# Kernel tuning notes

Hardware: AMD Instinct MI355X
Metric: run time of the kernel (lower is better)

Reference implementation:

```python
import jax, jax.numpy as jnp
import numpy as np

B, D, H, W = 16, 96, 96, 96
NUM_POINTS = 4096
THRESH = 0.5
CH = [3, 64, 128, 256, 512]   # shared-MLP channel progression (3 mlp layers + global_dim)
GROUPS = 8
EPS = 1e-5
HEAD_HIDDEN = 128


def setup_inputs() -> dict:
    key = jax.random.key(0)
    ks = jax.random.split(key, 8)
    inp = {"volume": jax.random.uniform(ks[0], (B, 1, D, H, W), jnp.float32)}
    for i in range(4):
        # Conv1d(kernel=1, no bias) weight (out, in); kaiming normal fan_out -> std=sqrt(2/out)
        inp[f"w{i+1}"] = jax.random.normal(ks[1 + i], (CH[i + 1], CH[i]), jnp.float32) * np.sqrt(2.0 / CH[i + 1]).astype(np.float32)
        inp[f"gn{i+1}_w"] = jnp.ones((CH[i + 1],), jnp.float32)
        inp[f"gn{i+1}_b"] = jnp.zeros((CH[i + 1],), jnp.float32)
    inp["fc1_w"] = jax.random.normal(ks[5], (HEAD_HIDDEN, CH[-1]), jnp.float32) * np.sqrt(2.0 / HEAD_HIDDEN).astype(np.float32)
    inp["fc1_b"] = jnp.zeros((HEAD_HIDDEN,), jnp.float32)
    inp["fc2_w"] = jax.random.normal(ks[6], (1, HEAD_HIDDEN), jnp.float32) * np.sqrt(2.0).astype(np.float32)
    inp["fc2_b"] = jnp.zeros((1,), jnp.float32)
    return inp


def volume_to_points(volume):
    """Batched, jit-safe version of volume_to_pointcloud (eval mode: linspace sampling)."""
    b, _, d, h, w = volume.shape
    mask = (volume[:, 0] > THRESH).reshape(b, -1)              # (B, D*H*W)
    n = mask.sum(axis=1)                                        # (B,) foreground counts
    # Stable argsort on ~mask puts foreground flat-indices first, in ascending order
    # == torch nonzero() ordering (row-major over D,H,W).
    order = jnp.argsort(jnp.logical_not(mask), axis=1, stable=True)  # (B, D*H*W)
    p = jnp.arange(NUM_POINTS)
    n_f = n.astype(jnp.float32)[:, None]
    # torch.linspace(0, n-1, P).long(): truncation toward zero
    lin = (p[None, :].astype(jnp.float32) * (n_f - 1.0) / (NUM_POINTS - 1)).astype(jnp.int32)
    lin = jnp.clip(lin, 0, jnp.maximum(n[:, None] - 1, 0))
    wrap = p[None, :] % jnp.maximum(n[:, None], 1)              # n < P fallback
    idx = jnp.where(n[:, None] >= NUM_POINTS, lin, wrap)        # (B, P)
    flat = jnp.take_along_axis(order, idx, axis=1)              # (B, P) flat voxel indices
    dd = flat // (h * w)
    hh = (flat // w) % h
    ww = flat % w
    coords = jnp.stack([dd, hh, ww], axis=1).astype(jnp.float32)  # (B, 3, P)
    scale = jnp.array([max(d - 1, 1), max(h - 1, 1), max(w - 1, 1)], jnp.float32)
    pts = coords / scale[None, :, None] * 2.0 - 1.0
    return jnp.where((n > 0)[:, None, None], pts, 0.0)


def group_norm(x, gamma, beta):
    b, c, npts = x.shape
    xg = x.reshape(b, GROUPS, c // GROUPS, npts)
    mu = xg.mean(axis=(2, 3), keepdims=True)
    var = xg.var(axis=(2, 3), keepdims=True)
    xn = ((xg - mu) * jax.lax.rsqrt(var + EPS)).reshape(b, c, npts)
    return xn * gamma[None, :, None] + beta[None, :, None]


def reference(volume, w1, gn1_w, gn1_b, w2, gn2_w, gn2_b, w3, gn3_w, gn3_b,
              w4, gn4_w, gn4_b, fc1_w, fc1_b, fc2_w, fc2_b):
    x = volume_to_points(volume)                                 # (B, 3, P)
    for cw, gw, gb in ((w1, gn1_w, gn1_b), (w2, gn2_w, gn2_b),
                       (w3, gn3_w, gn3_b), (w4, gn4_w, gn4_b)):
        x = jax.nn.relu(group_norm(jnp.einsum('oc,bcn->bon', cw, x), gw, gb))
    g = x.max(axis=2)                                            # (B, 512) global max-pool
    hdn = jax.nn.relu(g @ fc1_w.T + fc1_b)                       # dropout is identity in eval
    logits = (hdn @ fc2_w.T + fc2_b)[:, 0]                       # squeeze(-1) -> (B,)
    return logits
```

## Files before the change

kernel.cpp:

```cpp
#include <hip/hip_runtime.h>
#include <hip/hip_bf16.h>

#define NB 16
#define VOX 884736
#define NPTS 4096
#define CHUNK 1024
#define NCHUNK 864

typedef _Float16 f16x8 __attribute__((ext_vector_type(8)));
typedef _Float16 f16x4 __attribute__((ext_vector_type(4)));
typedef float f32x4 __attribute__((ext_vector_type(4)));

typedef const __attribute__((address_space(1))) _Float16 gf16;
typedef __attribute__((address_space(3))) _Float16 lf16;
#define GLOAD_LDS(gp, lp) __builtin_amdgcn_global_load_lds((gf16*)(gp), (lf16*)(lp), 16, 0, 0)

__device__ __forceinline__ f16x8 nrelu(f16x8 y, f16x8 sc, f16x8 sh) {
    f16x8 r = y * sc + sh;
    #pragma unroll
    for (int e = 0; e < 8; e++) r[e] = (r[e] > (_Float16)0.f) ? r[e] : (_Float16)0.f;
    return r;
}


__device__ inline void cast_chunk(const float* __restrict__ wf, _Float16* __restrict__ wh,
                                  int CIN, int t) {
    int lane = t & 63;
    int NCB = CIN / 32;
    int cb = (t >> 6) % NCB;
    int ob = t / (64 * NCB);
    int o = ob * 16 + (lane & 15);
    int c0 = cb * 32 + (lane >> 4) * 8;
    const float* src = wf + (size_t)o * CIN + c0;
    f16x8 v;
    #pragma unroll
    for (int e = 0; e < 8; e++) v[e] = (_Float16)src[e];
    *(f16x8*)(wh + (size_t)t * 8) = v;
}


__global__ __launch_bounds__(256) void count_cast_kernel(const float* __restrict__ vol,
                                                         int* __restrict__ counts,
                                                         unsigned long long* __restrict__ bits,
                                                         const float* __restrict__ w2,
                                                         const float* __restrict__ w3,
                                                         const float* __restrict__ w4,
                                                         _Float16* __restrict__ w2f,
                                                         _Float16* __restrict__ w3f,
                                                         _Float16* __restrict__ w4f) {
    if (blockIdx.x >= NB * NCHUNK) {
        int t = (blockIdx.x - NB * NCHUNK) * 256 + threadIdx.x;
        if (t < 1024) cast_chunk(w2, w2f, 64, t);
        else if (t < 1024 + 4096) cast_chunk(w3, w3f, 128, t - 1024);
        else if (t < 1024 + 4096 + 16384) cast_chunk(w4, w4f, 256, t - 5120);
        return;
    }
    int blk = blockIdx.x;
    const float4* v4 = (const float4*)(vol + (size_t)blk * CHUNK);
    float4 v = v4[threadIdx.x];
    int nib = (v.x > 0.5f) | ((v.y > 0.5f) << 1) | ((v.z > 0.5f) << 2) | ((v.w > 0.5f) << 3);
    __shared__ unsigned char nibs[256];
    nibs[threadIdx.x] = (unsigned char)nib;
    int cnt = __popc(nib);
    for (int off = 32; off; off >>= 1) cnt += __shfl_down(cnt, off, 64);
    __shared__ int s[4];
    if ((threadIdx.x & 63) == 0) s[threadIdx.x >> 6] = cnt;
    __syncthreads();
    if (threadIdx.x < 16) {
        unsigned long long wd = 0;
        #pragma unroll
        for (int i = 0; i < 16; i++)
            wd |= (unsigned long long)nibs[threadIdx.x * 16 + i] << (4 * i);
        bits[(size_t)blk * 16 + threadIdx.x] = wd;
    }
    if (threadIdx.x == 0) counts[blk] = s[0] + s[1] + s[2] + s[3];
}


__global__ __launch_bounds__(256) void points_kernel(const unsigned long long* __restrict__ bits,
                                                     const int* __restrict__ counts,
                                                     const float* __restrict__ w1,
                                                     float* __restrict__ pts,
                                                     float* __restrict__ pstat1) {
    int b = blockIdx.x >> 4;
    int pc = blockIdx.x & 15;
    int p = pc * 256 + threadIdx.x;
    int tid = threadIdx.x;
    __shared__ int sdat[NCHUNK];
    __shared__ float sw1[192];
    __shared__ int wsum[4];
    for (int i = tid; i < NCHUNK; i += 256) sdat[i] = counts[b * NCHUNK + i];
    if (tid < 192) sw1[tid] = w1[tid];
    __syncthreads();
    int i0 = tid * 4;
    int v0 = (i0 + 0 < NCHUNK) ? sdat[i0 + 0] : 0;
    int v1 = (i0 + 1 < NCHUNK) ? sdat[i0 + 1] : 0;
    int v2 = (i0 + 2 < NCHUNK) ? sdat[i0 + 2] : 0;
    int v3 = (i0 + 3 < NCHUNK) ? sdat[i0 + 3] : 0;
    int l3 = v0 + v1 + v2 + v3;
    int lane = tid & 63, wv = tid >> 6;
    int a = l3;
    #pragma unroll
    for (int off = 1; off < 64; off <<= 1) {
        int x = __shfl_up(a, off, 64);
        if (lane >= off) a += x;
    }
    if (lane == 63) wsum[wv] = a;
    __syncthreads();
    int woff = 0;
    #pragma unroll
    for (int w = 0; w < 4; w++) if (w < wv) woff += wsum[w];
    a += woff;
    int excl = a - l3;
    int n = wsum[0] + wsum[1] + wsum[2] + wsum[3];
    __syncthreads();
    if (i0 + 0 < NCHUNK) sdat[i0 + 0] = excl;
    if (i0 + 1 < NCHUNK) sdat[i0 + 1] = excl + v0;
    if (i0 + 2 < NCHUNK) sdat[i0 + 2] = excl + v0 + v1;
    if (i0 + 3 < NCHUNK) sdat[i0 + 3] = excl + v0 + v1 + v2;
    __syncthreads();
    float px = 0.f, py = 0.f, pz = 0.f;
    if (n > 0) {
        int k;
        if (n >= NPTS) {
            float t = (float)p * ((float)n - 1.0f);
            t = t / 4095.0f;
            k = (int)t;
            if (k > n - 1) k = n - 1;
            if (k < 0) k = 0;
        } else {
            k = p % n;
        }
        int lo = 0, hi = NCHUNK - 1;
        while (lo < hi) {
            int mid = (lo + hi + 1) >> 1;
            if (sdat[mid] <= k) lo = mid; else hi = mid - 1;
        }
        int rr = k - sdat[lo];
        const unsigned long long* wb = bits + ((size_t)b * NCHUNK + lo) * 16;
        unsigned long long chosen = 0;
        int wordidx = 0;
        bool found = false;
        #pragma unroll
        for (int w = 0; w < 16; w++) {
            unsigned long long m = wb[w];
            int pcnt = __popcll(m);
            bool take = (!found) && (rr < pcnt);
            if (take) { chosen = m; wordidx = w; found = true; }
            if (!found) rr -= pcnt;
        }
        int pos = 0;
        unsigned long long m64 = chosen;
        int c = __popcll(m64 & 0xFFFFFFFFull);
        if (rr >= c) { pos = 32; rr -= c; m64 >>= 32; }
        unsigned mm = (unsigned)m64;
        c = __popc(mm & 0xFFFFu); if (rr >= c) { pos += 16; rr -= c; mm >>= 16; }
        c = __popc(mm & 0xFFu);   if (rr >= c) { pos += 8;  rr -= c; mm >>= 8; }
        c = __popc(mm & 0xFu);    if (rr >= c) { pos += 4;  rr -= c; mm >>= 4; }
        c = __popc(mm & 0x3u);    if (rr >= c) { pos += 2;  rr -= c; mm >>= 2; }
        c = mm & 1u;              if (rr >= c) { pos += 1; }
        int flat = lo * CHUNK + wordidx * 64 + pos;
        int dd = flat / 9216;
        int rem = flat - dd * 9216;
        int hh = rem / 96;
        int ww = rem - hh * 96;
        px = (float)dd / 95.0f * 2.0f - 1.0f;
        py = (float)hh / 95.0f * 2.0f - 1.0f;
        pz = (float)ww / 95.0f * 2.0f - 1.0f;
    }
    pts[((size_t)b * 3 + 0) * NPTS + p] = px;
    pts[((size_t)b * 3 + 1) * NPTS + p] = py;
    pts[((size_t)b * 3 + 2) * NPTS + p] = pz;
    float s[8] = {}, q[8] = {};
    #pragma unroll
    for (int o = 0; o < 64; o++) {
        float av = sw1[o * 3 + 0] * px + sw1[o * 3 + 1] * py + sw1[o * 3 + 2] * pz;
        s[o >> 3] += av;
        q[o >> 3] += av * av;
    }
    __shared__ float red[4][8][2];
    #pragma unroll
    for (int g = 0; g < 8; g++) {
        float S = s[g], Q = q[g];
        for (int off = 32; off; off >>= 1) {
            S += __shfl_down(S, off, 64);
            Q += __shfl_down(Q, off, 64);
        }
        if ((threadIdx.x & 63) == 0) { red[wv][g][0] = S; red[wv][g][1] = Q; }
    }
    __syncthreads();
    if (tid < 8) {
        int g = tid;
        float S = red[0][g][0] + red[1][g][0] + red[2][g][0] + red[3][g][0];
        float Q = red[0][g][1] + red[1][g][1] + red[2][g][1] + red[3][g][1];
        float* d = pstat1 + (((size_t)(b * 8 + g)) * 16 + pc) * 2;
        d[0] = S; d[1] = Q;
    }
}


__global__ __launch_bounds__(256, 4) void fused_l2(const float* __restrict__ pts,
                                                   const float* __restrict__ w1,
                                                   const float* __restrict__ pstat1,
                                                   const float* __restrict__ gn1w,
                                                   const float* __restrict__ gn1b,
                                                   const _Float16* __restrict__ wfrag,
                                                   _Float16* __restrict__ y2,
                                                   float* __restrict__ pstat) {
    __shared__ _Float16 sl[64 * 64];
    __shared__ float sw1[192], ssc[64], ssh[64], ms1[8][2];
    int b = blockIdx.y, pblk = blockIdx.x, tid = threadIdx.x;
    if (tid < 192) sw1[tid] = w1[tid];
    if (tid < 8) {
        const float* pbase = pstat1 + (size_t)(b * 8 + tid) * 32;
        float S = 0.f, Q = 0.f;
        #pragma unroll
        for (int pc = 0; pc < 16; pc++) { S += pbase[2 * pc]; Q += pbase[2 * pc + 1]; }
        float inv = 1.0f / (8.0f * 4096.0f);
        float mu = S * inv;
        float var = Q * inv - mu * mu;
        if (var < 0.f) var = 0.f;
        ms1[tid][0] = mu; ms1[tid][1] = rsqrtf(var + 1e-5f);
    }
    __syncthreads();
    if (tid < 64) {
        int g = tid >> 3;
        float ga = gn1w[tid] * ms1[g][1];
        ssc[tid] = ga;
        ssh[tid] = gn1b[tid] - ms1[g][0] * ga;
    }
    __syncthreads();
    {
        int p = tid >> 2, qo = (tid & 3) * 16;
        int pg = pblk * 64 + p;
        float x0 = pts[((size_t)b * 3 + 0) * NPTS + pg];
        float x1 = pts[((size_t)b * 3 + 1) * NPTS + pg];
        float x2 = pts[((size_t)b * 3 + 2) * NPTS + pg];
        #pragma unroll
        for (int e = 0; e < 16; e++) {
            int o = qo + e;
            float a = sw1[o * 3 + 0] * x0 + sw1[o * 3 + 1] * x1 + sw1[o * 3 + 2] * x2;
            float r = fmaxf(a * ssc[o] + ssh[o], 0.f);
            sl[p * 64 + (((o >> 3) ^ (p & 7)) << 3) + (o & 7)] = (_Float16)r;
        }
    }
    __syncthreads();
    int wv = tid >> 6, lane = tid & 63, lr = lane & 15, lk = lane >> 4;
    int ph = wv & 1, oh = wv >> 1;
    int Pg = b * 64 + pblk;
    int pb32 = (Pg << 1) | ph;
    int P16 = Pg * 4 + ph * 2;
    f32x4 acc[2][4] = {};
    #pragma unroll
    for (int cb = 0; cb < 2; cb++) {
        int ch = cb * 4 + lk;
        f16x8 af0, af1;
        {
            int p0 = ph * 32 + lr;
            af0 = *(const f16x8*)(sl + p0 * 64 + ((ch ^ (p0 & 7)) << 3));
            int p1 = p0 + 16;
            af1 = *(const f16x8*)(sl + p1 * 64 + ((ch ^ (p1 & 7)) << 3));
        }
        #pragma unroll
        for (int i = 0; i < 4; i++) {
            int ofr = oh * 4 + i;
            f16x8 bf = *(const f16x8*)(wfrag + (((size_t)ofr * 2 + cb) * 64 + lane) * 8);
            acc[0][i] = __builtin_amdgcn_mfma_f32_16x16x32_f16(bf, af0, acc[0][i], 0, 0, 0);
            acc[1][i] = __builtin_amdgcn_mfma_f32_16x16x32_f16(bf, af1, acc[1][i], 0, 0, 0);
        }
    }
    #pragma unroll
    for (int i = 0; i < 4; i++) {
        int ofr = oh * 4 + i;
        int cb2 = ofr >> 1;
        int kg = (ofr & 1) * 2 + (lk >> 1);
        int lanep = lr + 16 * kg;
        int sub = lk & 1;
        #pragma unroll
        for (int pf = 0; pf < 2; pf++) {
            f16x4 vv;
            #pragma unroll
            for (int j = 0; j < 4; j++) vv[j] = (_Float16)acc[pf][i][j];
            *(f16x4*)(y2 + (((size_t)(P16 + pf) * 4 + cb2) * 64 + lanep) * 8 + sub * 4) = vv;
        }
        float s[4], q[4];
        #pragma unroll
        for (int j = 0; j < 4; j++) {
            float a0 = acc[0][i][j], a1 = acc[1][i][j];
            s[j] = a0 + a1; q[j] = a0 * a0 + a1 * a1;
        }
        #pragma unroll
        for (int m = 1; m <= 8; m <<= 1)
            #pragma unroll
            for (int j = 0; j < 4; j++) {
                s[j] += __shfl_xor(s[j], m, 64);
                q[j] += __shfl_xor(q[j], m, 64);
            }
        if (lr == 0) {
            int o0 = ofr * 16 + lk * 4;
            float* d = pstat + ((size_t)pb32 * 128 + o0) * 2;
            *(float4*)d = make_float4(s[0], q[0], s[1], q[1]);
            *(float4*)(d + 4) = make_float4(s[2], q[2], s[3], q[3]);
        }
    }
}


template <int C>
__global__ __launch_bounds__(256) void gn_finalizeG(const float* __restrict__ pstat,
                                                    const float* __restrict__ gamma,
                                                    const float* __restrict__ beta,
                                                    _Float16* __restrict__ scaleh,
                                                    _Float16* __restrict__ shifth) {
    constexpr int GS = C / 8;
    int b = blockIdx.x >> 3, g = blockIdx.x & 7;
    const float* base = pstat + (size_t)b * 128 * C * 2;
    float S = 0.f, Q = 0.f;
    for (int i = threadIdx.x; i < 128 * GS; i += 256) {
        int pb = i / GS;
        int c = g * GS + (i % GS);
        const float* d = base + ((size_t)pb * C + c) * 2;
        S += d[0]; Q += d[1];
    }
    for (int off = 32; off; off >>= 1) {
        S += __shfl_down(S, off, 64);
        Q += __shfl_down(Q, off, 64);
    }
    __shared__ float ss[8];
    if ((threadIdx.x & 63) == 0) {
        ss[(threadIdx.x >> 6) * 2] = S;
        ss[(threadIdx.x >> 6) * 2 + 1] = Q;
    }
    __syncthreads();
    __shared__ float ms[2];
    if (threadIdx.x == 0) {
        float St = ss[0] + ss[2] + ss[4] + ss[6];
        float Qt = ss[1] + ss[3] + ss[5] + ss[7];
        float inv = 1.0f / ((float)GS * 4096.0f);
        float mu = St * inv;
        float var = Qt * inv - mu * mu;
        if (var < 0.f) var = 0.f;
        ms[0] = mu; ms[1] = rsqrtf(var + 1e-5f);
    }
    __syncthreads();
    for (int i = threadIdx.x; i < GS; i += 256) {
        int c = g * GS + i;
        float ga = gamma[c] * ms[1];
        scaleh[(size_t)b * C + c] = (_Float16)ga;
        shifth[(size_t)b * C + c] = (_Float16)(beta[c] - ms[0] * ga);
    }
}


__global__ __launch_bounds__(256, 4) void fused_l3(const _Float16* __restrict__ y2,
                                                   const _Float16* __restrict__ sch,
                                                   const _Float16* __restrict__ shh,
                                                   const _Float16* __restrict__ w3f,
                                                   _Float16* __restrict__ y3,
                                                   float* __restrict__ pstatOut) {
    __shared__ _Float16 sl[64 * 128];
    __shared__ _Float16 sscf[128], sshf[128];
    int b = blockIdx.y, pblk = blockIdx.x, tid = threadIdx.x;
    int wv = tid >> 6, lane = tid & 63, lr = lane & 15, lk = lane >> 4;
    int Pg = b * 64 + pblk;
    const _Float16* yt = y2 + (size_t)Pg * 64 * 128;
    #pragma unroll
    for (int i = 0; i < 4; i++) {
        int off = (wv * 4 + i) * 512;
        GLOAD_LDS(yt + off + lane * 8, sl + off);
    }
    if (tid < 128) {
        sscf[tid] = sch[b * 128 + tid];
        sshf[tid] = shh[b * 128 + tid];
    }
    __syncthreads();
    #pragma unroll
    for (int k = 0; k < 4; k++) {
        int q = tid + k * 256;
        int ln = q & 63;
        int cb = (q >> 6) & 3;
        int c0 = cb * 32 + (ln >> 4) * 8;
        f16x8 v = *(const f16x8*)(sl + (size_t)q * 8);
        f16x8 scv = *(const f16x8*)(sscf + c0);
        f16x8 shv = *(const f16x8*)(sshf + c0);
        *(f16x8*)(sl + (size_t)q * 8) = nrelu(v, scv, shv);
    }
    __syncthreads();
    int ph = wv & 1, oh = wv >> 1;
    int pb32 = (Pg << 1) | ph;
    int P16 = Pg * 4 + ph * 2;
    f16x8 af[2][4];
    #pragma unroll
    for (int cb = 0; cb < 4; cb++) {
        af[0][cb] = *(const f16x8*)(sl + (((ph * 2 + 0) * 4 + cb) * 64 + lane) * 8);
        af[1][cb] = *(const f16x8*)(sl + (((ph * 2 + 1) * 4 + cb) * 64 + lane) * 8);
    }
    #pragma unroll
    for (int ck = 0; ck < 2; ck++) {
        f32x4 acc[2][4] = {};
        #pragma unroll
        for (int cb = 0; cb < 4; cb++) {
            #pragma unroll
            for (int i = 0; i < 4; i++) {
                int ofr = oh * 8 + ck * 4 + i;
                f16x8 bf = *(const f16x8*)(w3f + (((size_t)ofr * 4 + cb) * 64 + lane) * 8);
                acc[0][i] = __builtin_amdgcn_mfma_f32_16x16x32_f16(bf, af[0][cb], acc[0][i], 0, 0, 0);
                acc[1][i] = __builtin_amdgcn_mfma_f32_16x16x32_f16(bf, af[1][cb], acc[1][i], 0, 0, 0);
            }
        }
        #pragma unroll
        for (int i = 0; i < 4; i++) {
            int ofr = oh * 8 + ck * 4 + i;
            int cb3 = ofr >> 1;
            int kg = (ofr & 1) * 2 + (lk >> 1);
            int lanep = lr + 16 * kg;
            int sub = lk & 1;
            #pragma unroll
            for (int pf = 0; pf < 2; pf++) {
                f16x4 vv;
                #pragma unroll
                for (int j = 0; j < 4; j++) vv[j] = (_Float16)acc[pf][i][j];
                *(f16x4*)(y3 + (((size_t)(P16 + pf) * 8 + cb3) * 64 + lanep) * 8 + sub * 4) = vv;
            }
            float s[4], q[4];
            #pragma unroll
            for (int j = 0; j < 4; j++) {
                float a0 = acc[0][i][j], a1 = acc[1][i][j];
                s[j] = a0 + a1; q[j] = a0 * a0 + a1 * a1;
            }
            #pragma unroll
            for (int m = 1; m <= 8; m <<= 1)
                #pragma unroll
                for (int j = 0; j < 4; j++) {
                    s[j] += __shfl_xor(s[j], m, 64);
                    q[j] += __shfl_xor(q[j], m, 64);
                }
            if (lr == 0) {
                int o0 = ofr * 16 + lk * 4;
                float* d = pstatOut + ((size_t)pb32 * 256 + o0) * 2;
                *(float4*)d = make_float4(s[0], q[0], s[1], q[1]);
                *(float4*)(d + 4) = make_float4(s[2], q[2], s[3], q[3]);
            }
        }
    }
}


__global__ __launch_bounds__(256, 4) void fused_l4(const _Float16* __restrict__ y3,
                                                   const _Float16* __restrict__ sch,
                                                   const _Float16* __restrict__ shh,
                                                   const _Float16* __restrict__ w4f,
                                                   float* __restrict__ pstat4) {
    __shared__ _Float16 sl[64 * 256];
    __shared__ _Float16 sscf[256], sshf[256];
    int b = blockIdx.y, pblk = blockIdx.x, tid = threadIdx.x;
    int wv = tid >> 6, lane = tid & 63, lr = lane & 15, lk = lane >> 4;
    int Pg = b * 64 + pblk;
    const _Float16* yt = y3 + (size_t)Pg * 64 * 256;
    #pragma unroll
    for (int i = 0; i < 8; i++) {
        int off = (wv * 8 + i) * 512;
        GLOAD_LDS(yt + off + lane * 8, sl + off);
    }
    sscf[tid] = sch[b * 256 + tid];
    sshf[tid] = shh[b * 256 + tid];
    __syncthreads();
    #pragma unroll
    for (int k = 0; k < 8; k++) {
        int q = tid + k * 256;
        int ln = q & 63;
        int cb = (q >> 6) & 7;
        int c0 = cb * 32 + (ln >> 4) * 8;
        f16x8 v = *(const f16x8*)(sl + (size_t)q * 8);
        f16x8 scv = *(const f16x8*)(sscf + c0);
        f16x8 shv = *(const f16x8*)(sshf + c0);
        *(f16x8*)(sl + (size_t)q * 8) = nrelu(v, scv, shv);
    }
    __syncthreads();
    int ph = wv & 1, oh = wv >> 1;
    int pb32 = (Pg << 1) | ph;
    f16x8 af[2][8];
    #pragma unroll
    for (int cb = 0; cb < 8; cb++) {
        af[0][cb] = *(const f16x8*)(sl + (((ph * 2 + 0) * 8 + cb) * 64 + lane) * 8);
        af[1][cb] = *(const f16x8*)(sl + (((ph * 2 + 1) * 8 + cb) * 64 + lane) * 8);
    }
    #pragma unroll
    for (int ck = 0; ck < 4; ck++) {
        f32x4 acc[2][4] = {};
        #pragma unroll
        for (int cb = 0; cb < 8; cb++) {
            #pragma unroll
            for (int i = 0; i < 4; i++) {
                int ofr = oh * 16 + ck * 4 + i;
                f16x8 bf = *(const f16x8*)(w4f + (((size_t)ofr * 8 + cb) * 64 + lane) * 8);
                acc[0][i] = __builtin_amdgcn_mfma_f32_16x16x32_f16(af[0][cb], bf, acc[0][i], 0, 0, 0);
                acc[1][i] = __builtin_amdgcn_mfma_f32_16x16x32_f16(af[1][cb], bf, acc[1][i], 0, 0, 0);
            }
        }
        #pragma unroll
        for (int i = 0; i < 4; i++) {
            int ofr = oh * 16 + ck * 4 + i;
            float S = 0.f, Q = 0.f, MX = -1e30f, MN = 1e30f;
            #pragma unroll
            for (int pf = 0; pf < 2; pf++)
                #pragma unroll
                for (int j = 0; j < 4; j++) {
                    float v = acc[pf][i][j];
                    S += v; Q += v * v;
                    MX = fmaxf(MX, v); MN = fminf(MN, v);
                }
            S += __shfl_xor(S, 16, 64); Q += __shfl_xor(Q, 16, 64);
            MX = fmaxf(MX, __shfl_xor(MX, 16, 64)); MN = fminf(MN, __shfl_xor(MN, 16, 64));
            S += __shfl_xor(S, 32, 64); Q += __shfl_xor(Q, 32, 64);
            MX = fmaxf(MX, __shfl_xor(MX, 32, 64)); MN = fminf(MN, __shfl_xor(MN, 32, 64));
            if (lk == 0) {
                int o = ofr * 16 + lr;
                *(float4*)(pstat4 + ((size_t)pb32 * 512 + o) * 4) = make_float4(S, Q, MX, MN);
            }
        }
    }
}


__global__ __launch_bounds__(256) void pool_final(const float* __restrict__ pstat4,
                                                  const float* __restrict__ gamma,
                                                  const float* __restrict__ beta,
                                                  float* __restrict__ g) {
    int b = blockIdx.x >> 3, gr = blockIdx.x & 7;
    int ch = threadIdx.x & 63;
    int pg = threadIdx.x >> 6;
    int o = gr * 64 + ch;
    float S = 0.f, Q = 0.f, MX = -1e30f, MN = 1e30f;
    for (int pb = pg; pb < 128; pb += 4) {
        float4 v = *(const float4*)(pstat4 + (((size_t)(b * 128 + pb)) * 512 + o) * 4);
        S += v.x; Q += v.y; MX = fmaxf(MX, v.z); MN = fminf(MN, v.w);
    }
    __shared__ float sS[4][64], sQ[4][64], sMX[4][64], sMN[4][64];
    sS[pg][ch] = S; sQ[pg][ch] = Q; sMX[pg][ch] = MX; sMN[pg][ch] = MN;
    __syncthreads();
    if (threadIdx.x < 64) {
        float Sc = sS[0][ch] + sS[1][ch] + sS[2][ch] + sS[3][ch];
        float Qc = sQ[0][ch] + sQ[1][ch] + sQ[2][ch] + sQ[3][ch];
        float MXc = fmaxf(fmaxf(sMX[0][ch], sMX[1][ch]), fmaxf(sMX[2][ch], sMX[3][ch]));
        float MNc = fminf(fminf(sMN[0][ch], sMN[1][ch]), fminf(sMN[2][ch], sMN[3][ch]));
        float St = Sc, Qt = Qc;
        for (int off = 32; off; off >>= 1) {
            St += __shfl_xor(St, off, 64);
            Qt += __shfl_xor(Qt, off, 64);
        }
        float inv = 1.0f / (64.0f * 4096.0f);
        float mu = St * inv;
        float var = Qt * inv - mu * mu;
        if (var < 0.f) var = 0.f;
        float rstd = rsqrtf(var + 1e-5f);
        float sc = gamma[o] * rstd;
        float sh = beta[o] - mu * sc;
        float m = (sc >= 0.f ? MXc : MNc) * sc + sh;
        g[b * 512 + o] = fmaxf(m, 0.f);
    }
}


__global__ __launch_bounds__(128) void head_kernel(const float* __restrict__ g,
                                                   const float* __restrict__ fc1w,
                                                   const float* __restrict__ fc1b,
                                                   const float* __restrict__ fc2w,
                                                   const float* __restrict__ fc2b,
                                                   float* __restrict__ out) {
    int b = blockIdx.x;
    int o = threadIdx.x;
    __shared__ float sg[512];
    for (int i = threadIdx.x; i < 512; i += 128) sg[i] = g[b * 512 + i];
    __syncthreads();
    float acc = fc1b[o];
    for (int c = 0; c < 512; c++) acc += sg[c] * fc1w[o * 512 + c];
    float h = fmaxf(acc, 0.f) * fc2w[o];
    for (int off = 32; off; off >>= 1) h += __shfl_down(h, off, 64);
    __shared__ float s2[2];
    if ((threadIdx.x & 63) == 0) s2[threadIdx.x >> 6] = h;
    __syncthreads();
    if (threadIdx.x == 0) out[b] = s2[0] + s2[1] + fc2b[0];
}


extern "C" void kernel_launch(void* const* d_in, const int* in_sizes, int n_in,
                              void* d_out, int out_size, void* d_ws, size_t ws_size,
                              hipStream_t stream) {
    const float* vol  = (const float*)d_in[0];
    const float* w1   = (const float*)d_in[1];
    const float* gn1w = (const float*)d_in[2];
    const float* gn1b = (const float*)d_in[3];
    const float* w2   = (const float*)d_in[4];
    const float* gn2w = (const float*)d_in[5];
    const float* gn2b = (const float*)d_in[6];
    const float* w3   = (const float*)d_in[7];
    const float* gn3w = (const float*)d_in[8];
    const float* gn3b = (const float*)d_in[9];
    const float* w4   = (const float*)d_in[10];
    const float* gn4w = (const float*)d_in[11];
    const float* gn4b = (const float*)d_in[12];
    const float* fc1w = (const float*)d_in[13];
    const float* fc1b = (const float*)d_in[14];
    const float* fc2w = (const float*)d_in[15];
    const float* fc2b = (const float*)d_in[16];
    float* out = (float*)d_out;

    char* ws = (char*)d_ws;
    size_t cur = 0;
    auto alloc = [&](size_t bytes) -> void* {
        cur = (cur + 255) & ~(size_t)255;
        void* p = ws + cur;
        cur += bytes;
        return p;
    };
    int*      counts  = (int*)alloc((size_t)NB * NCHUNK * 4);
    unsigned long long* bits = (unsigned long long*)alloc((size_t)NB * NCHUNK * 16 * 8);
    float*    pts     = (float*)alloc((size_t)NB * 3 * NPTS * 4);
    float*    gbuf    = (float*)alloc((size_t)NB * 512 * 4);
    float*    pstat1  = (float*)alloc((size_t)NB * 8 * 16 * 2 * 4);
    float*    pstatG  = (float*)alloc((size_t)NB * 128 * 128 * 2 * 4);
    float*    pstatG2 = (float*)alloc((size_t)NB * 128 * 256 * 2 * 4);
    float*    pstat4  = (float*)alloc((size_t)NB * 128 * 512 * 4 * 4);
    _Float16* sc2h    = (_Float16*)alloc((size_t)NB * 128 * 2);
    _Float16* sh2h    = (_Float16*)alloc((size_t)NB * 128 * 2);
    _Float16* sc3h    = (_Float16*)alloc((size_t)NB * 256 * 2);
    _Float16* sh3h    = (_Float16*)alloc((size_t)NB * 256 * 2);
    _Float16* w2f     = (_Float16*)alloc((size_t)128 * 64 * 2);
    _Float16* w3f     = (_Float16*)alloc((size_t)256 * 128 * 2);
    _Float16* w4f     = (_Float16*)alloc((size_t)512 * 256 * 2);
    _Float16* y2      = (_Float16*)alloc((size_t)NB * NPTS * 128 * 2);
    _Float16* y3      = (_Float16*)alloc((size_t)NB * NPTS * 256 * 2);

    count_cast_kernel<<<dim3(NB * NCHUNK + 84), dim3(256), 0, stream>>>(
        vol, counts, bits, w2, w3, w4, w2f, w3f, w4f);

    points_kernel<<<dim3(NB * 16), dim3(256), 0, stream>>>(bits, counts, w1, pts, pstat1);

    fused_l2<<<dim3(64, NB), dim3(256), 0, stream>>>(pts, w1, pstat1, gn1w, gn1b, w2f, y2, pstatG);

    gn_finalizeG<128><<<dim3(NB * 8), dim3(256), 0, stream>>>(pstatG, gn2w, gn2b, sc2h, sh2h);
    fused_l3<<<dim3(64, NB), dim3(256), 0, stream>>>(y2, sc2h, sh2h, w3f, y3, pstatG2);

    gn_finalizeG<256><<<dim3(NB * 8), dim3(256), 0, stream>>>(pstatG2, gn3w, gn3b, sc3h, sh3h);
    fused_l4<<<dim3(64, NB), dim3(256), 0, stream>>>(y3, sc3h, sh3h, w4f, pstat4);

    pool_final<<<dim3(NB * 8), dim3(256), 0, stream>>>(pstat4, gn4w, gn4b, gbuf);
    head_kernel<<<dim3(NB), dim3(128), 0, stream>>>(gbuf, fc1w, fc1b, fc2w, fc2b, out);
}
```

Before: 128.6 us.

## Restructure layer-4 GEMM to stream double-buffered weights through LDS per wave

fused_l4 now has each wave own 32 points, held as normalized activations in registers loaded straight from global memory. The 512x256 weight matrix is streamed through a double-buffered LDS tile in 16 chunks using async global-to-LDS loads, so all four waves share each weight tile. The grid is halved to 32 blocks per batch. fused_l3 also loads its A fragments inside the cb loop instead of hoisting them, which lowers register pressure. This adds a barrier per chunk and means fewer blocks in flight.

Measured after the change: 123.9 us. 1.04x faster.

```diff
diff --git a/kernel.cpp b/kernel.cpp
--- a/kernel.cpp
+++ b/kernel.cpp
@@ -389,23 +389,19 @@
     int ph = wv & 1, oh = wv >> 1;
     int pb32 = (Pg << 1) | ph;
     int P16 = Pg * 4 + ph * 2;
-    f16x8 af[2][4];
-    #pragma unroll
-    for (int cb = 0; cb < 4; cb++) {
-        af[0][cb] = *(const f16x8*)(sl + (((ph * 2 + 0) * 4 + cb) * 64 + lane) * 8);
-        af[1][cb] = *(const f16x8*)(sl + (((ph * 2 + 1) * 4 + cb) * 64 + lane) * 8);
-    }
     #pragma unroll
     for (int ck = 0; ck < 2; ck++) {
         f32x4 acc[2][4] = {};
         #pragma unroll
         for (int cb = 0; cb < 4; cb++) {
+            f16x8 af0 = *(const f16x8*)(sl + (((ph * 2 + 0) * 4 + cb) * 64 + lane) * 8);
+            f16x8 af1 = *(const f16x8*)(sl + (((ph * 2 + 1) * 4 + cb) * 64 + lane) * 8);
             #pragma unroll
             for (int i = 0; i < 4; i++) {
                 int ofr = oh * 8 + ck * 4 + i;
                 f16x8 bf = *(const f16x8*)(w3f + (((size_t)ofr * 4 + cb) * 64 + lane) * 8);
-                acc[0][i] = __builtin_amdgcn_mfma_f32_16x16x32_f16(bf, af[0][cb], acc[0][i], 0, 0, 0);
-                acc[1][i] = __builtin_amdgcn_mfma_f32_16x16x32_f16(bf, af[1][cb], acc[1][i], 0, 0, 0);
+                acc[0][i] = __builtin_amdgcn_mfma_f32_16x16x32_f16(bf, af0, acc[0][i], 0, 0, 0);
+                acc[1][i] = __builtin_amdgcn_mfma_f32_16x16x32_f16(bf, af1, acc[1][i], 0, 0, 0);
             }
         }
         #pragma unroll
@@ -451,56 +447,55 @@
                                                    const _Float16* __restrict__ shh,
                                                    const _Float16* __restrict__ w4f,
                                                    float* __restrict__ pstat4) {
-    __shared__ _Float16 sl[64 * 256];
+    __shared__ _Float16 wbuf[2][8192];
     __shared__ _Float16 sscf[256], sshf[256];
     int b = blockIdx.y, pblk = blockIdx.x, tid = threadIdx.x;
     int wv = tid >> 6, lane = tid & 63, lr = lane & 15, lk = lane >> 4;
-    int Pg = b * 64 + pblk;
-    const _Float16* yt = y3 + (size_t)Pg * 64 * 256;
-    #pragma unroll
-    for (int i = 0; i < 8; i++) {
-        int off = (wv * 8 + i) * 512;
-        GLOAD_LDS(yt + off + lane * 8, sl + off);
+    #pragma unroll
+    for (int i = 0; i < 4; i++) {
+        int off = (wv * 4 + i) * 512;
+        GLOAD_LDS(w4f + off + lane * 8, &wbuf[0][0] + off);
     }
     sscf[tid] = sch[b * 256 + tid];
     sshf[tid] = shh[b * 256 + tid];
     __syncthreads();
-    #pragma unroll
-    for (int k = 0; k < 8; k++) {
-        int q = tid + k * 256;
-        int ln = q & 63;
-        int cb = (q >> 6) & 7;
-        int c0 = cb * 32 + (ln >> 4) * 8;
-        f16x8 v = *(const f16x8*)(sl + (size_t)q * 8);
-        f16x8 scv = *(const f16x8*)(sscf + c0);
-        f16x8 shv = *(const f16x8*)(sshf + c0);
-        *(f16x8*)(sl + (size_t)q * 8) = nrelu(v, scv, shv);
-    }
-    __syncthreads();
-    int ph = wv & 1, oh = wv >> 1;
-    int pb32 = (Pg << 1) | ph;
+    int P16 = (b * NPTS + pblk * 128 + wv * 32) >> 4;
+    int pb32 = (b * NPTS + pblk * 128 + wv * 32) >> 5;
     f16x8 af[2][8];
     #pragma unroll
-    for (int cb = 0; cb < 8; cb++) {
-        af[0][cb] = *(const f16x8*)(sl + (((ph * 2 + 0) * 8 + cb) * 64 + lane) * 8);
-        af[1][cb] = *(const f16x8*)(sl + (((ph * 2 + 1) * 8 + cb) * 64 + lane) * 8);
-    }
-    #pragma unroll
-    for (int ck = 0; ck < 4; ck++) {
-        f32x4 acc[2][4] = {};
+    for (int pf = 0; pf < 2; pf++)
         #pragma unroll
         for (int cb = 0; cb < 8; cb++) {
+            f16x8 v = *(const f16x8*)(y3 + (((size_t)(P16 + pf) * 8 + cb) * 64 + lane) * 8);
+            f16x8 scv = *(const f16x8*)(sscf + cb * 32 + lk * 8);
+            f16x8 shv = *(const f16x8*)(sshf + cb * 32 + lk * 8);
+            af[pf][cb] = nrelu(v, scv, shv);
+        }
+    #pragma unroll
+    for (int ck = 0; ck < 16; ck++) {
+        if (ck < 15) {
+            const _Float16* src = w4f + (size_t)(ck + 1) * 8192;
+            _Float16* dst = &wbuf[(ck + 1) & 1][0];
             #pragma unroll
             for (int i = 0; i < 4; i++) {
-                int ofr = oh * 16 + ck * 4 + i;
-                f16x8 bf = *(const f16x8*)(w4f + (((size_t)ofr * 8 + cb) * 64 + lane) * 8);
+                int off = (wv * 4 + i) * 512;
+                GLOAD_LDS(src + off + lane * 8, dst + off);
+            }
+        }
+        const _Float16* wb = &wbuf[ck & 1][0];
+        f32x4 acc[2][2] = {};
+        #pragma unroll
+        for (int cb = 0; cb < 8; cb++) {
+            #pragma unroll
+            for (int i = 0; i < 2; i++) {
+                f16x8 bf = *(const f16x8*)(wb + ((i * 8 + cb) * 64 + lane) * 8);
                 acc[0][i] = __builtin_amdgcn_mfma_f32_16x16x32_f16(af[0][cb], bf, acc[0][i], 0, 0, 0);
                 acc[1][i] = __builtin_amdgcn_mfma_f32_16x16x32_f16(af[1][cb], bf, acc[1][i], 0, 0, 0);
             }
         }
         #pragma unroll
-        for (int i = 0; i < 4; i++) {
-            int ofr = oh * 16 + ck * 4 + i;
+        for (int i = 0; i < 2; i++) {
+            int ofr = ck * 2 + i;
             float S = 0.f, Q = 0.f, MX = -1e30f, MN = 1e30f;
             #pragma unroll
             for (int pf = 0; pf < 2; pf++)
@@ -519,6 +514,7 @@
                 *(float4*)(pstat4 + ((size_t)pb32 * 512 + o) * 4) = make_float4(S, Q, MX, MN);
             }
         }
+        __syncthreads();
     }
 }
 
@@ -643,7 +639,7 @@
     fused_l3<<<dim3(64, NB), dim3(256), 0, stream>>>(y2, sc2h, sh2h, w3f, y3, pstatG2);
 
     gn_finalizeG<256><<<dim3(NB * 8), dim3(256), 0, stream>>>(pstatG2, gn3w, gn3b, sc3h, sh3h);
-    fused_l4<<<dim3(64, NB), dim3(256), 0, stream>>>(y3, sc3h, sh3h, w4f, pstat4);
+    fused_l4<<<dim3(32, NB), dim3(256), 0, stream>>>(y3, sc3h, sh3h, w4f, pstat4);
 
     pool_final<<<dim3(NB * 8), dim3(256), 0, stream>>>(pstat4, gn4w, gn4b, gbuf);
     head_kernel<<<dim3(NB), dim3(128), 0, stream>>>(gbuf, fc1w, fc1b, fc2w, fc2b, out);
```
